# Kernel tuning notes

Hardware: AMD Instinct MI355X
Metric: run time of the kernel (lower is better)

## Reference

```python
import jax, jax.numpy as jnp
import numpy as np

B, NUM_CAMS, C, N_ANCHOR = 1, 6, 256, 900
NUM_LEVELS, NUM_FIXED, NUM_LEARN, NUM_GROUPS = 4, 7, 6, 8
NUM_PTS = NUM_FIXED + NUM_LEARN
IMG_W, IMG_H = 704, 256
SHAPES = [(64, 176), (32, 88), (16, 44), (8, 22)]  # strides 4,8,16,32


def setup_inputs() -> dict:
    key = jax.random.key(0)
    ks = jax.random.split(key, 12)
    sum_hw = sum(h * w for h, w in SHAPES)
    feature = jax.random.normal(ks[0], (B, NUM_CAMS, sum_hw, C), jnp.float32)
    spatial_shapes = jnp.array(SHAPES, dtype=jnp.int32)
    starts = np.cumsum([0] + [h * w for h, w in SHAPES[:-1]])
    level_start_index = jnp.array(starts, dtype=jnp.int32)
    # anchor: [x,y,z, log(w),log(l),log(h), sin(yaw), cos(yaw), vx,vy,vz]
    center = jax.random.uniform(ks[1], (B, N_ANCHOR, 3), minval=-40.0, maxval=40.0) * jnp.array([1.0, 1.0, 0.05])
    size = jnp.log(jnp.array([2.0, 4.5, 1.7])) * jnp.ones((B, N_ANCHOR, 3))
    yaw = jax.random.uniform(ks[2], (B, N_ANCHOR, 1), minval=-np.pi, maxval=np.pi)
    anchor = jnp.concatenate([center, size, jnp.sin(yaw), jnp.cos(yaw), jnp.zeros((B, N_ANCHOR, 3))], axis=-1).astype(jnp.float32)
    instance_feature = jax.random.normal(ks[3], (B, N_ANCHOR, C), jnp.float32)
    time_interval = jnp.full((B,), 0.5, jnp.float32)
    # plausible lidar2img = K @ [R|t] for 6 surround cameras
    l2i = []
    for c in range(NUM_CAMS):
        a = 2.0 * np.pi * c / NUM_CAMS
        Rz = np.array([[np.cos(a), -np.sin(a), 0.0], [np.sin(a), np.cos(a), 0.0], [0.0, 0.0, 1.0]])
        swap = np.array([[0.0, -1.0, 0.0], [0.0, 0.0, -1.0], [1.0, 0.0, 0.0]])  # lidar axes -> camera axes
        Rcam = swap @ Rz.T
        t = -Rcam @ np.array([0.0, 0.0, 1.5])
        E = np.eye(4); E[:3, :3] = Rcam; E[:3, 3] = t
        K = np.eye(4); K[0, 0] = K[1, 1] = 400.0; K[0, 2] = IMG_W / 2.0; K[1, 2] = IMG_H / 2.0
        l2i.append(K @ E)
    lidar2img = jnp.asarray(np.broadcast_to(np.stack(l2i)[None], (B, NUM_CAMS, 4, 4)), jnp.float32)
    image_wh = jnp.broadcast_to(jnp.array([IMG_W, IMG_H], jnp.float32), (B, NUM_CAMS, 2))
    s = 0.02
    n_w = NUM_CAMS * NUM_LEVELS * NUM_PTS * NUM_GROUPS
    return dict(
        instance_feature=instance_feature, anchor=anchor, time_interval=time_interval,
        feature=feature, spatial_shapes=spatial_shapes, level_start_index=level_start_index,
        lidar2img=lidar2img, image_wh=image_wh,
        enc_w=jax.random.normal(ks[4], (11, C)) * s, enc_b=jnp.zeros((C,), jnp.float32),
        kp_fixed=jax.random.normal(ks[5], (NUM_FIXED, 3)) * 0.5,
        kp_w=jax.random.normal(ks[6], (C, NUM_LEARN * 3)) * s, kp_b=jnp.zeros((NUM_LEARN * 3,), jnp.float32),
        wfc_w=jax.random.normal(ks[7], (C, n_w)) * s, wfc_b=jnp.zeros((n_w,), jnp.float32),
        out_w=jax.random.normal(ks[8], (C, C)) * s, out_b=jnp.zeros((C,), jnp.float32),
    )


def _bilinear_sample(feature, spatial_shapes, level_start_index, pts, valid):
    # feature: [B,Cm,sumHW,C]; pts: [B,Cm,N,P,2] normalized to [0,1]; valid: [B,Cm,N,P]
    Bn, Cm, _, Cd = feature.shape
    N, P = pts.shape[2], pts.shape[3]
    per_level = []
    for l in range(NUM_LEVELS):
        H = spatial_shapes[l, 0]
        W = spatial_shapes[l, 1]
        start = level_start_index[l]
        # grid_sample align_corners=False convention
        x = pts[..., 0] * W - 0.5
        y = pts[..., 1] * H - 0.5
        x0f = jnp.floor(x); y0f = jnp.floor(y)
        wx = (x - x0f)[..., None]
        wy = (y - y0f)[..., None]
        x0 = x0f.astype(jnp.int32); y0 = y0f.astype(jnp.int32)

        def gather(xi, yi):
            ok = (xi >= 0) & (xi < W) & (yi >= 0) & (yi < H) & valid
            xi_c = jnp.clip(xi, 0, W - 1)
            yi_c = jnp.clip(yi, 0, H - 1)
            idx = (start + yi_c * W + xi_c).reshape(Bn, Cm, N * P, 1)
            g = jnp.take_along_axis(feature, idx, axis=2).reshape(Bn, Cm, N, P, Cd)
            return g * ok[..., None]

        v = (gather(x0, y0) * (1 - wx) * (1 - wy)
             + gather(x0 + 1, y0) * wx * (1 - wy)
             + gather(x0, y0 + 1) * (1 - wx) * wy
             + gather(x0 + 1, y0 + 1) * wx * wy)
        per_level.append(v)
    return jnp.stack(per_level, axis=4)  # [B,Cm,N,P,L,C]


def _forward(instance_feature, anchor, feature, spatial_shapes, level_start_index,
             lidar2img, image_wh, enc_w, enc_b, kp_fixed, kp_w, kp_b, wfc_w, wfc_b, out_w, out_b):
    Bn, N, Cd = instance_feature.shape
    anchor_embed = anchor @ enc_w + enc_b                      # anchor_encoder
    # --- keypoint generation (7 fixed + 6 learnable), scaled by box size, rotated by yaw ---
    center = anchor[..., :3]
    size = jnp.exp(anchor[..., 3:6])
    sin_y, cos_y = anchor[..., 6:7], anchor[..., 7:8]
    learn = (instance_feature @ kp_w + kp_b).reshape(Bn, N, NUM_LEARN, 3)
    offs = jnp.concatenate([jnp.broadcast_to(kp_fixed, (Bn, N, NUM_FIXED, 3)), learn], axis=2)
    offs = offs * size[:, :, None, :]
    ox, oy, oz = offs[..., 0], offs[..., 1], offs[..., 2]
    rx = cos_y * ox - sin_y * oy
    ry = sin_y * ox + cos_y * oy
    kp = jnp.stack([rx, ry, oz], axis=-1) + center[:, :, None, :]          # [B,N,P,3]
    # --- project to each camera ---
    kp_h = jnp.concatenate([kp, jnp.ones_like(kp[..., :1])], axis=-1)
    p = jnp.einsum('bcij,bnpj->bcnpi', lidar2img, kp_h)                    # [B,Cm,N,P,4]
    depth = p[..., 2]
    xy = p[..., :2] / jnp.clip(depth, 1e-5, None)[..., None]
    pts = xy / image_wh[:, :, None, None, :]                               # [0,1] normalized
    valid = depth > 1e-5
    # --- multi-scale multi-camera bilinear gather ---
    feats = _bilinear_sample(feature, spatial_shapes, level_start_index, pts, valid)  # [B,Cm,N,P,L,C]
    # --- group-wise attention weights, softmax over cams*levels*pts ---
    w = ((instance_feature + anchor_embed) @ wfc_w + wfc_b).reshape(Bn, N, -1, NUM_GROUPS)
    w = jax.nn.softmax(w, axis=-2).reshape(Bn, N, NUM_CAMS, NUM_LEVELS, NUM_PTS, NUM_GROUPS)
    f = jnp.transpose(feats, (0, 2, 1, 4, 3, 5)).reshape(
        Bn, N, NUM_CAMS, NUM_LEVELS, NUM_PTS, NUM_GROUPS, Cd // NUM_GROUPS)
    agg = jnp.sum(f * w[..., None], axis=(2, 3, 4)).reshape(Bn, N, Cd)
    return instance_feature + (agg @ out_w + out_b)


def reference(instance_feature, anchor, time_interval, feature, spatial_shapes, level_start_index,
              lidar2img, image_wh, enc_w, enc_b, kp_fixed, kp_w, kp_b, wfc_w, wfc_b, out_w, out_b):
    # time_interval is only consumed by the 'refine' op, which is not in the executed op list
    return _forward(instance_feature, anchor, feature, spatial_shapes, level_start_index,
                    lidar2img, image_wh, enc_w, enc_b, kp_fixed, kp_w, kp_b, wfc_w, wfc_b, out_w, out_b)
```

## Files before the change

kernel.cpp:

```cpp
#include <hip/hip_runtime.h>
#include <math.h>

#define N_ANCHOR   900
#define NUM_CAMS   6
#define CDIM       256
#define NUM_LEVELS 4
#define NUM_FIXED  7
#define NUM_LEARN  6
#define NUM_PTS    13
#define NUM_GROUPS 8
#define NW         2496
#define NI         312
#define SUM_HW     14960
#define MAXJOBS    1248

typedef short short8 __attribute__((ext_vector_type(8)));
typedef float floatx4 __attribute__((ext_vector_type(4)));

__device__ __forceinline__ unsigned short f2bf(float x) {
  unsigned u = __float_as_uint(x);
  u += 0x7FFFu + ((u >> 16) & 1u);
  return (unsigned short)(u >> 16);
}

__global__ __launch_bounds__(256) void k_pre(
    const float* __restrict__ inst, const float* __restrict__ anchor,
    const float* __restrict__ l2i, const float* __restrict__ image_wh,
    const float* __restrict__ kp_fixed, const float* __restrict__ kp_w,
    const float* __restrict__ kp_b,
    const float* __restrict__ enc_w, const float* __restrict__ enc_b,
    const float* __restrict__ wfc_w,
    unsigned short* __restrict__ qbf, unsigned short* __restrict__ wbf_t,
    float* __restrict__ pts_out, float* __restrict__ valid_out) {
  const int t = threadIdx.x;

  if (blockIdx.x >= N_ANCHOR) {
    const int bi = blockIdx.x - N_ANCHOR;
    const int n0 = (bi % 39) * 64, k0 = (bi / 39) * 64;
    __shared__ float tile[64][65];
    #pragma unroll
    for (int i = 0; i < 4; ++i) {
      const int kr = (t >> 4) + i * 16;
      const int nc = (t & 15) * 4;
      const float4 v = *(const float4*)&wfc_w[(size_t)(k0 + kr) * NW + n0 + nc];
      tile[kr][nc + 0] = v.x; tile[kr][nc + 1] = v.y;
      tile[kr][nc + 2] = v.z; tile[kr][nc + 3] = v.w;
    }
    __syncthreads();
    #pragma unroll
    for (int i = 0; i < 4; ++i) {
      const int nr = (t >> 4) + i * 16;
      const int kc = (t & 15) * 4;
      ushort4 o;
      o.x = f2bf(tile[kc + 0][nr]);
      o.y = f2bf(tile[kc + 1][nr]);
      o.z = f2bf(tile[kc + 2][nr]);
      o.w = f2bf(tile[kc + 3][nr]);
      *(ushort4*)&wbf_t[(size_t)(n0 + nr) * CDIM + k0 + kc] = o;
    }
    return;
  }

  const int n = blockIdx.x;
  __shared__ float anc[11];
  __shared__ float learn[NUM_LEARN * 3];
  __shared__ float psum[8][NUM_LEARN * 3];
  __shared__ float kps[NUM_PTS][3];
  __shared__ float ins[CDIM];

  const float iv = inst[n * CDIM + t];
  ins[t] = iv;
  if (t < 11) anc[t] = anchor[n * 11 + t];
  __syncthreads();

  {
    float s = enc_b[t] + iv;
    #pragma unroll
    for (int k = 0; k < 11; ++k) s += anc[k] * enc_w[k * CDIM + t];
    qbf[n * CDIM + t] = f2bf(s);
  }

  if (t < 144) {
    const int c = t / 18, j = t % 18;
    float s = 0.0f;
    const int k0 = c * 32;
    #pragma unroll
    for (int k = 0; k < 32; ++k)
      s += ins[k0 + k] * kp_w[(k0 + k) * (NUM_LEARN * 3) + j];
    psum[c][j] = s;
  }
  __syncthreads();
  if (t < NUM_LEARN * 3) {
    float s = kp_b[t];
    #pragma unroll
    for (int c = 0; c < 8; ++c) s += psum[c][t];
    learn[t] = s;
  }
  __syncthreads();

  if (t < NUM_PTS) {
    const float sx = expf(anc[3]), sy = expf(anc[4]), sz = expf(anc[5]);
    float ox, oy, oz;
    if (t < NUM_FIXED) {
      ox = kp_fixed[t * 3 + 0]; oy = kp_fixed[t * 3 + 1]; oz = kp_fixed[t * 3 + 2];
    } else {
      const int j = (t - NUM_FIXED) * 3;
      ox = learn[j + 0]; oy = learn[j + 1]; oz = learn[j + 2];
    }
    ox *= sx; oy *= sy; oz *= sz;
    const float sn = anc[6], cs = anc[7];
    kps[t][0] = cs * ox - sn * oy + anc[0];
    kps[t][1] = sn * ox + cs * oy + anc[1];
    kps[t][2] = oz + anc[2];
  }
  __syncthreads();

  if (t < NUM_CAMS * NUM_PTS) {
    const int cam = t / NUM_PTS, p = t % NUM_PTS;
    const float* M = l2i + cam * 16;
    const float kx = kps[p][0], ky = kps[p][1], kz = kps[p][2];
    const float px = M[0] * kx + M[1] * ky + M[2]  * kz + M[3];
    const float py = M[4] * kx + M[5] * ky + M[6]  * kz + M[7];
    const float pz = M[8] * kx + M[9] * ky + M[10] * kz + M[11];
    const float d = fmaxf(pz, 1e-5f);
    const float u = (px / d) / image_wh[cam * 2 + 0];
    const float v = (py / d) / image_wh[cam * 2 + 1];
    const int o = n * NUM_CAMS * NUM_PTS + t;
    pts_out[o * 2 + 0] = u;
    pts_out[o * 2 + 1] = v;
    valid_out[o] = (pz > 1e-5f) ? 1.0f : 0.0f;
  }
}

__global__ __launch_bounds__(256) void k_wgemm(
    const unsigned short* __restrict__ qbf,
    const unsigned short* __restrict__ wbf_t,
    const float* __restrict__ wfc_b, float* __restrict__ raw) {
  const int tid = threadIdx.x;
  const int w = tid >> 6;
  const int l = tid & 63;
  const int n0 = blockIdx.x * 64;
  const int m0 = blockIdx.y * 64;
  __shared__ unsigned short Bs[64 * 64];

  floatx4 acc[4];
  #pragma unroll
  for (int s = 0; s < 4; ++s) acc[s] = (floatx4){0.f, 0.f, 0.f, 0.f};

  const int arow = m0 + w * 16 + (l & 15);
  const bool arow_ok = arow < N_ANCHOR;
  const unsigned short* aptr = qbf + (size_t)arow * CDIM + (l >> 4) * 8;

  for (int k0 = 0; k0 < CDIM; k0 += 64) {
    #pragma unroll
    for (int i = 0; i < 2; ++i) {
      const int idx = tid + i * 256;
      const int n = idx >> 3, kg = idx & 7;
      const short8 bv =
          *(const short8*)&wbf_t[(size_t)(n0 + n) * CDIM + k0 + kg * 8];
      *(short8*)&Bs[n * 64 + ((kg ^ (n & 7)) * 8)] = bv;
    }
    __syncthreads();
    #pragma unroll
    for (int c = 0; c < 2; ++c) {
      short8 a = (short8){0, 0, 0, 0, 0, 0, 0, 0};
      if (arow_ok) a = *(const short8*)&aptr[k0 + c * 32];
      #pragma unroll
      for (int s = 0; s < 4; ++s) {
        const int nloc = s * 16 + (l & 15);
        const int k8 = c * 4 + (l >> 4);
        const short8 b = *(const short8*)&Bs[nloc * 64 + ((k8 ^ (nloc & 7)) * 8)];
        acc[s] = __builtin_amdgcn_mfma_f32_16x16x32_bf16(a, b, acc[s], 0, 0, 0);
      }
    }
    __syncthreads();
  }

  const int colb = n0 + (l & 15);
  const int rowb = m0 + w * 16 + (l >> 4) * 4;
  #pragma unroll
  for (int s = 0; s < 4; ++s) {
    const int col = colb + s * 16;
    const float bias = wfc_b[col];
    #pragma unroll
    for (int r = 0; r < 4; ++r) {
      const int row = rowb + r;
      if (row < N_ANCHOR)
        raw[(size_t)row * NW + col] = acc[s][r] + bias;
    }
  }
}

__global__ __launch_bounds__(1024) void k_mega(
    const float* __restrict__ feature,
    const int* __restrict__ spatial_shapes, const int* __restrict__ level_start,
    const float* __restrict__ pts, const float* __restrict__ valid,
    const float* __restrict__ raw,
    const float* __restrict__ inst,
    const float* __restrict__ out_w, const float* __restrict__ out_b,
    float* __restrict__ out) {
  const int n = blockIdx.x;
  const int t = threadIdx.x;
  const int wv = t >> 6;
  const int lane = t & 63;
  const int g = lane >> 3;

  __shared__ float w_row[NW];
  __shared__ float uv_s[NUM_CAMS * NUM_PTS][2];
  __shared__ float val_s[NUM_CAMS * NUM_PTS];
  __shared__ float mx_s[NUM_GROUPS], inv_s[NUM_GROUPS];
  __shared__ int shp[NUM_LEVELS][2];
  __shared__ int lst[NUM_LEVELS];
  __shared__ int joff[MAXJOBS];
  __shared__ float jcf[MAXJOBS];
  __shared__ int jw_s[MAXJOBS];
  __shared__ int njobs;
  __shared__ float4 red4[16][64];
  __shared__ float a_s[CDIM];
  __shared__ float red2[4][CDIM];

  {
    const float4* src = (const float4*)(raw + (size_t)n * NW);
    for (int j = t; j < NW / 4; j += 1024) *(float4*)&w_row[j * 4] = src[j];
  }
  if (t < NUM_CAMS * NUM_PTS) {
    const int o = n * NUM_CAMS * NUM_PTS + t;
    uv_s[t][0] = pts[o * 2 + 0];
    uv_s[t][1] = pts[o * 2 + 1];
    val_s[t] = valid[o];
  }
  if (t < NUM_LEVELS) {
    shp[t][0] = spatial_shapes[t * 2 + 0];
    shp[t][1] = spatial_shapes[t * 2 + 1];
    lst[t] = level_start[t];
  }
  if (t == 0) njobs = 0;
  __syncthreads();

  if (t < 256) {
    const int sg = t >> 5, sl = t & 31;
    float m = -1e30f;
    for (int i = sl; i < NI; i += 32) m = fmaxf(m, w_row[i * NUM_GROUPS + sg]);
    #pragma unroll
    for (int o = 16; o > 0; o >>= 1) m = fmaxf(m, __shfl_down(m, o, 32));
    m = __shfl(m, 0, 32);
    float s = 0.0f;
    for (int i = sl; i < NI; i += 32) s += expf(w_row[i * NUM_GROUPS + sg] - m);
    #pragma unroll
    for (int o = 16; o > 0; o >>= 1) s += __shfl_down(s, o, 32);
    if (sl == 0) { mx_s[sg] = m; inv_s[sg] = 1.0f / s; }
  }

  for (int jt = t; jt < MAXJOBS; jt += 1024) {
    const int cam = jt / 208;
    const int r = jt % 208;
    const int q = r / 52;
    const int pl = r % 52;
    const int p = pl >> 2, l = pl & 3;
    if (val_s[cam * NUM_PTS + p] != 0.0f) {
      const int H = shp[l][0], W = shp[l][1], st = lst[l];
      const float x = uv_s[cam * NUM_PTS + p][0] * (float)W - 0.5f;
      const float y = uv_s[cam * NUM_PTS + p][1] * (float)H - 0.5f;
      const float x0f = floorf(x), y0f = floorf(y);
      const float wx = x - x0f, wy = y - y0f;
      const int dx = q & 1, dy = q >> 1;
      const int xx = (int)x0f + dx;
      const int yy = (int)y0f + dy;
      if (xx >= 0 && xx < W && yy >= 0 && yy < H) {
        const int pos = atomicAdd(&njobs, 1);
        joff[pos] = (cam * SUM_HW + st + yy * W + xx) * CDIM;
        jcf[pos] = (dx ? wx : 1.0f - wx) * (dy ? wy : 1.0f - wy);
        jw_s[pos] = (cam * 52 + l * NUM_PTS + p) * 8;
      }
    }
  }
  __syncthreads();

  const int nj = njobs;
  const int padded = (nj + 31) & ~31;
  for (int j = nj + t; j < padded; j += 1024) {
    joff[j] = 0; jcf[j] = 0.0f; jw_s[j] = 0;
  }
  for (int j = t; j < NW; j += 1024)
    w_row[j] = expf(w_row[j] - mx_s[j & 7]) * inv_s[j & 7];
  __syncthreads();

  float4 acc = make_float4(0.f, 0.f, 0.f, 0.f);
  const int cio = lane * 4;
  for (int j = wv; j < padded; j += 32) {
    const int o0 = joff[j];
    const float wg0 = jcf[j] * w_row[jw_s[j] + g];
    const float4 f0 = *(const float4*)&feature[o0 + cio];
    const int j1 = j + 16;
    const int o1 = joff[j1];
    const float wg1 = jcf[j1] * w_row[jw_s[j1] + g];
    const float4 f1 = *(const float4*)&feature[o1 + cio];
    acc.x += wg0 * f0.x + wg1 * f1.x;
    acc.y += wg0 * f0.y + wg1 * f1.y;
    acc.z += wg0 * f0.z + wg1 * f1.z;
    acc.w += wg0 * f0.w + wg1 * f1.w;
  }
  red4[wv][lane] = acc;
  __syncthreads();

  if (t < 64) {
    float4 s = red4[0][t];
    #pragma unroll
    for (int w = 1; w < 16; ++w) {
      const float4 b = red4[w][t];
      s.x += b.x; s.y += b.y; s.z += b.z; s.w += b.w;
    }
    *(float4*)&a_s[t * 4] = s;
  }
  __syncthreads();

  {
    const int col = t & 255, ks = t >> 8;
    float p = 0.0f;
    const int k0 = ks * 64;
    #pragma unroll
    for (int k = 0; k < 64; ++k)
      p += a_s[k0 + k] * out_w[(k0 + k) * CDIM + col];
    red2[ks][col] = p;
  }
  __syncthreads();
  if (t < CDIM) {
    const float s = red2[0][t] + red2[1][t] + red2[2][t] + red2[3][t];
    out[(size_t)n * CDIM + t] = s + out_b[t] + inst[(size_t)n * CDIM + t];
  }
}

extern "C" void kernel_launch(void* const* d_in, const int* in_sizes, int n_in,
                              void* d_out, int out_size, void* d_ws, size_t ws_size,
                              hipStream_t stream) {
  const float* inst           = (const float*)d_in[0];
  const float* anchor         = (const float*)d_in[1];
  const float* feature        = (const float*)d_in[3];
  const int*   spatial_shapes = (const int*)d_in[4];
  const int*   level_start    = (const int*)d_in[5];
  const float* l2i            = (const float*)d_in[6];
  const float* image_wh       = (const float*)d_in[7];
  const float* enc_w          = (const float*)d_in[8];
  const float* enc_b          = (const float*)d_in[9];
  const float* kp_fixed       = (const float*)d_in[10];
  const float* kp_w           = (const float*)d_in[11];
  const float* kp_b           = (const float*)d_in[12];
  const float* wfc_w          = (const float*)d_in[13];
  const float* wfc_b          = (const float*)d_in[14];
  const float* out_w          = (const float*)d_in[15];
  const float* out_b          = (const float*)d_in[16];

  float* ws    = (float*)d_ws;
  float* pts   = ws;
  float* valid = pts + N_ANCHOR * NUM_CAMS * NUM_PTS * 2;
  float* wbuf  = valid + N_ANCHOR * NUM_CAMS * NUM_PTS;
  unsigned short* qbf   = (unsigned short*)(wbuf + (size_t)N_ANCHOR * NW);
  unsigned short* wbf_t = qbf + N_ANCHOR * CDIM;

  k_pre<<<N_ANCHOR + 156, 256, 0, stream>>>(
      inst, anchor, l2i, image_wh, kp_fixed, kp_w, kp_b, enc_w, enc_b,
      wfc_w, qbf, wbf_t, pts, valid);
  k_wgemm<<<dim3(NW / 64, (N_ANCHOR + 63) / 64), 256, 0, stream>>>(
      qbf, wbf_t, wfc_b, wbuf);
  k_mega<<<N_ANCHOR, 1024, 0, stream>>>(
      feature, spatial_shapes, level_start, pts, valid, wbuf,
      inst, out_w, out_b, (float*)d_out);
}
```

Measured before the change: 209.6 us.

## Split output projection into bf16 MFMA GEMM kernel and slim gather kernel

Moves the per-anchor output projection out of the gather kernel into a separate bf16 MFMA GEMM. The per-anchor fp32 GEMV re-read out_w in every block, and the GEMM removes that traffic. The gather kernel drops to 512 threads, stores softmax weights group-major for conflict-free access, compacts jobs with wave ballot instead of per-thread atomics, and unrolls the gather four-wide. The costs are an extra launch, an intermediate bf16 buffer and reduced precision in the projection.

```diff
diff --git a/kernel.cpp b/kernel.cpp
--- a/kernel.cpp
+++ b/kernel.cpp
@@ -13,6 +13,7 @@
 #define NI         312
 #define SUM_HW     14960
 #define MAXJOBS    1248
+#define WSTRIDE    328
 
 typedef short short8 __attribute__((ext_vector_type(8)));
 typedef float floatx4 __attribute__((ext_vector_type(4)));
@@ -29,20 +30,23 @@
     const float* __restrict__ kp_fixed, const float* __restrict__ kp_w,
     const float* __restrict__ kp_b,
     const float* __restrict__ enc_w, const float* __restrict__ enc_b,
-    const float* __restrict__ wfc_w,
+    const float* __restrict__ wfc_w, const float* __restrict__ out_w,
     unsigned short* __restrict__ qbf, unsigned short* __restrict__ wbf_t,
+    unsigned short* __restrict__ owt,
     float* __restrict__ pts_out, float* __restrict__ valid_out) {
   const int t = threadIdx.x;
 
   if (blockIdx.x >= N_ANCHOR) {
     const int bi = blockIdx.x - N_ANCHOR;
-    const int n0 = (bi % 39) * 64, k0 = (bi / 39) * 64;
+    const float* src; unsigned short* dst; int ss, n0, k0;
+    if (bi < 156) { src = wfc_w; dst = wbf_t; ss = NW;   n0 = (bi % 39) * 64; k0 = (bi / 39) * 64; }
+    else { const int b2 = bi - 156; src = out_w; dst = owt; ss = CDIM; n0 = (b2 % 4) * 64; k0 = (b2 / 4) * 64; }
     __shared__ float tile[64][65];
     #pragma unroll
     for (int i = 0; i < 4; ++i) {
       const int kr = (t >> 4) + i * 16;
       const int nc = (t & 15) * 4;
-      const float4 v = *(const float4*)&wfc_w[(size_t)(k0 + kr) * NW + n0 + nc];
+      const float4 v = *(const float4*)&src[(size_t)(k0 + kr) * ss + n0 + nc];
       tile[kr][nc + 0] = v.x; tile[kr][nc + 1] = v.y;
       tile[kr][nc + 2] = v.z; tile[kr][nc + 3] = v.w;
     }
@@ -56,7 +60,7 @@
       o.y = f2bf(tile[kc + 1][nr]);
       o.z = f2bf(tile[kc + 2][nr]);
       o.w = f2bf(tile[kc + 3][nr]);
-      *(ushort4*)&wbf_t[(size_t)(n0 + nr) * CDIM + k0 + kc] = o;
+      *(ushort4*)&dst[(size_t)(n0 + nr) * CDIM + k0 + kc] = o;
     }
     return;
   }
@@ -191,21 +195,19 @@
   }
 }
 
-__global__ __launch_bounds__(1024) void k_mega(
+__global__ __launch_bounds__(512) void k_mega(
     const float* __restrict__ feature,
     const int* __restrict__ spatial_shapes, const int* __restrict__ level_start,
     const float* __restrict__ pts, const float* __restrict__ valid,
     const float* __restrict__ raw,
-    const float* __restrict__ inst,
-    const float* __restrict__ out_w, const float* __restrict__ out_b,
-    float* __restrict__ out) {
+    unsigned short* __restrict__ abf) {
   const int n = blockIdx.x;
   const int t = threadIdx.x;
   const int wv = t >> 6;
   const int lane = t & 63;
   const int g = lane >> 3;
 
-  __shared__ float w_row[NW];
+  __shared__ float w_rowT[NUM_GROUPS * WSTRIDE];
   __shared__ float uv_s[NUM_CAMS * NUM_PTS][2];
   __shared__ float val_s[NUM_CAMS * NUM_PTS];
   __shared__ float mx_s[NUM_GROUPS], inv_s[NUM_GROUPS];
@@ -213,15 +215,21 @@
   __shared__ int lst[NUM_LEVELS];
   __shared__ int joff[MAXJOBS];
   __shared__ float jcf[MAXJOBS];
-  __shared__ int jw_s[MAXJOBS];
+  __shared__ short jw_s[MAXJOBS];
   __shared__ int njobs;
-  __shared__ float4 red4[16][64];
-  __shared__ float a_s[CDIM];
-  __shared__ float red2[4][CDIM];
+  __shared__ float4 red4[8][64];
 
   {
     const float4* src = (const float4*)(raw + (size_t)n * NW);
-    for (int j = t; j < NW / 4; j += 1024) *(float4*)&w_row[j * 4] = src[j];
+    for (int j4 = t; j4 < NW / 4; j4 += 512) {
+      const float4 v = src[j4];
+      const int i = j4 >> 1;
+      const int gb = (j4 & 1) * 4;
+      w_rowT[(gb + 0) * WSTRIDE + i] = v.x;
+      w_rowT[(gb + 1) * WSTRIDE + i] = v.y;
+      w_rowT[(gb + 2) * WSTRIDE + i] = v.z;
+      w_rowT[(gb + 3) * WSTRIDE + i] = v.w;
+    }
   }
   if (t < NUM_CAMS * NUM_PTS) {
     const int o = n * NUM_CAMS * NUM_PTS + t;
@@ -237,68 +245,87 @@
   if (t == 0) njobs = 0;
   __syncthreads();
 
-  if (t < 256) {
-    const int sg = t >> 5, sl = t & 31;
+  {
+    const float* wr = &w_rowT[wv * WSTRIDE];
     float m = -1e30f;
-    for (int i = sl; i < NI; i += 32) m = fmaxf(m, w_row[i * NUM_GROUPS + sg]);
-    #pragma unroll
-    for (int o = 16; o > 0; o >>= 1) m = fmaxf(m, __shfl_down(m, o, 32));
-    m = __shfl(m, 0, 32);
+    for (int i = lane; i < NI; i += 64) m = fmaxf(m, wr[i]);
+    #pragma unroll
+    for (int o = 32; o > 0; o >>= 1) m = fmaxf(m, __shfl_down(m, o, 64));
+    m = __shfl(m, 0, 64);
     float s = 0.0f;
-    for (int i = sl; i < NI; i += 32) s += expf(w_row[i * NUM_GROUPS + sg] - m);
-    #pragma unroll
-    for (int o = 16; o > 0; o >>= 1) s += __shfl_down(s, o, 32);
-    if (sl == 0) { mx_s[sg] = m; inv_s[sg] = 1.0f / s; }
-  }
-
-  for (int jt = t; jt < MAXJOBS; jt += 1024) {
-    const int cam = jt / 208;
-    const int r = jt % 208;
-    const int q = r / 52;
-    const int pl = r % 52;
-    const int p = pl >> 2, l = pl & 3;
-    if (val_s[cam * NUM_PTS + p] != 0.0f) {
-      const int H = shp[l][0], W = shp[l][1], st = lst[l];
-      const float x = uv_s[cam * NUM_PTS + p][0] * (float)W - 0.5f;
-      const float y = uv_s[cam * NUM_PTS + p][1] * (float)H - 0.5f;
-      const float x0f = floorf(x), y0f = floorf(y);
-      const float wx = x - x0f, wy = y - y0f;
-      const int dx = q & 1, dy = q >> 1;
-      const int xx = (int)x0f + dx;
-      const int yy = (int)y0f + dy;
-      if (xx >= 0 && xx < W && yy >= 0 && yy < H) {
-        const int pos = atomicAdd(&njobs, 1);
-        joff[pos] = (cam * SUM_HW + st + yy * W + xx) * CDIM;
-        jcf[pos] = (dx ? wx : 1.0f - wx) * (dy ? wy : 1.0f - wy);
-        jw_s[pos] = (cam * 52 + l * NUM_PTS + p) * 8;
+    for (int i = lane; i < NI; i += 64) s += expf(wr[i] - m);
+    #pragma unroll
+    for (int o = 32; o > 0; o >>= 1) s += __shfl_down(s, o, 64);
+    if (lane == 0) { mx_s[wv] = m; inv_s[wv] = 1.0f / s; }
+  }
+
+  #pragma unroll
+  for (int base = 0; base < MAXJOBS; base += 512) {
+    const int jt = base + t;
+    bool ok = false;
+    int off = 0; short wbi = 0; float cf = 0.0f;
+    if (jt < MAXJOBS) {
+      const int cam = jt / 208;
+      const int r = jt % 208;
+      const int q = r / 52;
+      const int pl = r % 52;
+      const int p = pl >> 2, l = pl & 3;
+      if (val_s[cam * NUM_PTS + p] != 0.0f) {
+        const int H = shp[l][0], W = shp[l][1], st = lst[l];
+        const float x = uv_s[cam * NUM_PTS + p][0] * (float)W - 0.5f;
+        const float y = uv_s[cam * NUM_PTS + p][1] * (float)H - 0.5f;
+        const float x0f = floorf(x), y0f = floorf(y);
+        const float wx = x - x0f, wy = y - y0f;
+        const int dx = q & 1, dy = q >> 1;
+        const int xx = (int)x0f + dx;
+        const int yy = (int)y0f + dy;
+        if (xx >= 0 && xx < W && yy >= 0 && yy < H) {
+          ok = true;
+          off = (cam * SUM_HW + st + yy * W + xx) * CDIM;
+          cf = (dx ? wx : 1.0f - wx) * (dy ? wy : 1.0f - wy);
+          wbi = (short)(cam * 52 + l * NUM_PTS + p);
+        }
       }
+    }
+    const unsigned long long mask = __ballot(ok);
+    const int cnt = __popcll(mask);
+    int wbase = 0;
+    if (lane == 0 && cnt) wbase = atomicAdd(&njobs, cnt);
+    wbase = __shfl(wbase, 0, 64);
+    if (ok) {
+      const int pos = wbase + __popcll(mask & ((1ull << lane) - 1ull));
+      joff[pos] = off; jcf[pos] = cf; jw_s[pos] = wbi;
     }
   }
   __syncthreads();
 
   const int nj = njobs;
   const int padded = (nj + 31) & ~31;
-  for (int j = nj + t; j < padded; j += 1024) {
+  for (int j = nj + t; j < padded; j += 512) {
     joff[j] = 0; jcf[j] = 0.0f; jw_s[j] = 0;
   }
-  for (int j = t; j < NW; j += 1024)
-    w_row[j] = expf(w_row[j] - mx_s[j & 7]) * inv_s[j & 7];
+  for (int e = t; e < NUM_GROUPS * WSTRIDE; e += 512) {
+    const int gg = e / WSTRIDE;
+    w_rowT[e] = expf(w_rowT[e] - mx_s[gg]) * inv_s[gg];
+  }
   __syncthreads();
 
   float4 acc = make_float4(0.f, 0.f, 0.f, 0.f);
   const int cio = lane * 4;
   for (int j = wv; j < padded; j += 32) {
-    const int o0 = joff[j];
-    const float wg0 = jcf[j] * w_row[jw_s[j] + g];
-    const float4 f0 = *(const float4*)&feature[o0 + cio];
-    const int j1 = j + 16;
-    const int o1 = joff[j1];
-    const float wg1 = jcf[j1] * w_row[jw_s[j1] + g];
-    const float4 f1 = *(const float4*)&feature[o1 + cio];
-    acc.x += wg0 * f0.x + wg1 * f1.x;
-    acc.y += wg0 * f0.y + wg1 * f1.y;
-    acc.z += wg0 * f0.z + wg1 * f1.z;
-    acc.w += wg0 * f0.w + wg1 * f1.w;
+    float4 f[4]; float wg[4];
+    #pragma unroll
+    for (int i = 0; i < 4; ++i) {
+      const int jj = j + i * 8;
+      const int o = joff[jj];
+      wg[i] = jcf[jj] * w_rowT[g * WSTRIDE + jw_s[jj]];
+      f[i] = *(const float4*)&feature[o + cio];
+    }
+    #pragma unroll
+    for (int i = 0; i < 4; ++i) {
+      acc.x += wg[i] * f[i].x; acc.y += wg[i] * f[i].y;
+      acc.z += wg[i] * f[i].z; acc.w += wg[i] * f[i].w;
+    }
   }
   red4[wv][lane] = acc;
   __syncthreads();
@@ -306,27 +333,74 @@
   if (t < 64) {
     float4 s = red4[0][t];
     #pragma unroll
-    for (int w = 1; w < 16; ++w) {
+    for (int w = 1; w < 8; ++w) {
       const float4 b = red4[w][t];
       s.x += b.x; s.y += b.y; s.z += b.z; s.w += b.w;
     }
-    *(float4*)&a_s[t * 4] = s;
-  }
-  __syncthreads();
-
-  {
-    const int col = t & 255, ks = t >> 8;
-    float p = 0.0f;
-    const int k0 = ks * 64;
-    #pragma unroll
-    for (int k = 0; k < 64; ++k)
-      p += a_s[k0 + k] * out_w[(k0 + k) * CDIM + col];
-    red2[ks][col] = p;
-  }
-  __syncthreads();
-  if (t < CDIM) {
-    const float s = red2[0][t] + red2[1][t] + red2[2][t] + red2[3][t];
-    out[(size_t)n * CDIM + t] = s + out_b[t] + inst[(size_t)n * CDIM + t];
+    ushort4 o;
+    o.x = f2bf(s.x); o.y = f2bf(s.y); o.z = f2bf(s.z); o.w = f2bf(s.w);
+    *(ushort4*)&abf[(size_t)n * CDIM + t * 4] = o;
+  }
+}
+
+__global__ __launch_bounds__(256) void k_ogemm(
+    const unsigned short* __restrict__ abf,
+    const unsigned short* __restrict__ owt,
+    const float* __restrict__ out_b, const float* __restrict__ inst,
+    float* __restrict__ out) {
+  const int tid = threadIdx.x;
+  const int w = tid >> 6;
+  const int l = tid & 63;
+  const int n0 = blockIdx.x * 64;
+  const int m0 = blockIdx.y * 64;
+  __shared__ unsigned short Bs[64 * 64];
+
+  floatx4 acc[4];
+  #pragma unroll
+  for (int s = 0; s < 4; ++s) acc[s] = (floatx4){0.f, 0.f, 0.f, 0.f};
+
+  const int arow = m0 + w * 16 + (l & 15);
+  const bool arow_ok = arow < N_ANCHOR;
+  const unsigned short* aptr = abf + (size_t)arow * CDIM + (l >> 4) * 8;
+
+  for (int k0 = 0; k0 < CDIM; k0 += 64) {
+    #pragma unroll
+    for (int i = 0; i < 2; ++i) {
+      const int idx = tid + i * 256;
+      const int n = idx >> 3, kg = idx & 7;
+      const short8 bv =
+          *(const short8*)&owt[(size_t)(n0 + n) * CDIM + k0 + kg * 8];
+      *(short8*)&Bs[n * 64 + ((kg ^ (n & 7)) * 8)] = bv;
+    }
+    __syncthreads();
+    #pragma unroll
+    for (int c = 0; c < 2; ++c) {
+      short8 a = (short8){0, 0, 0, 0, 0, 0, 0, 0};
+      if (arow_ok) a = *(const short8*)&aptr[k0 + c * 32];
+      #pragma unroll
+      for (int s = 0; s < 4; ++s) {
+        const int nloc = s * 16 + (l & 15);
+        const int k8 = c * 4 + (l >> 4);
+        const short8 b = *(const short8*)&Bs[nloc * 64 + ((k8 ^ (nloc & 7)) * 8)];
+        acc[s] = __builtin_amdgcn_mfma_f32_16x16x32_bf16(a, b, acc[s], 0, 0, 0);
+      }
+    }
+    __syncthreads();
+  }
+
+  const int colb = n0 + (l & 15);
+  const int rowb = m0 + w * 16 + (l >> 4) * 4;
+  #pragma unroll
+  for (int s = 0; s < 4; ++s) {
+    const int col = colb + s * 16;
+    const float bias = out_b[col];
+    #pragma unroll
+    for (int r = 0; r < 4; ++r) {
+      const int row = rowb + r;
+      if (row < N_ANCHOR)
+        out[(size_t)row * CDIM + col] =
+            acc[s][r] + bias + inst[(size_t)row * CDIM + col];
+    }
   }
 }
 
@@ -356,13 +430,16 @@
   float* wbuf  = valid + N_ANCHOR * NUM_CAMS * NUM_PTS;
   unsigned short* qbf   = (unsigned short*)(wbuf + (size_t)N_ANCHOR * NW);
   unsigned short* wbf_t = qbf + N_ANCHOR * CDIM;
-
-  k_pre<<<N_ANCHOR + 156, 256, 0, stream>>>(
+  unsigned short* owt   = wbf_t + (size_t)NW * CDIM;
+  unsigned short* abf   = owt + CDIM * CDIM;
+
+  k_pre<<<N_ANCHOR + 156 + 16, 256, 0, stream>>>(
       inst, anchor, l2i, image_wh, kp_fixed, kp_w, kp_b, enc_w, enc_b,
-      wfc_w, qbf, wbf_t, pts, valid);
+      wfc_w, out_w, qbf, wbf_t, owt, pts, valid);
   k_wgemm<<<dim3(NW / 64, (N_ANCHOR + 63) / 64), 256, 0, stream>>>(
       qbf, wbf_t, wfc_b, wbuf);
-  k_mega<<<N_ANCHOR, 1024, 0, stream>>>(
-      feature, spatial_shapes, level_start, pts, valid, wbuf,
-      inst, out_w, out_b, (float*)d_out);
-}
+  k_mega<<<N_ANCHOR, 512, 0, stream>>>(
+      feature, spatial_shapes, level_start, pts, valid, wbuf, abf);
+  k_ogemm<<<dim3(CDIM / 64, (N_ANCHOR + 63) / 64), 256, 0, stream>>>(
+      abf, owt, out_b, inst, (float*)d_out);
+}
```

Measured after the change: 198.1 us. 1.06x faster.
